# Kernel tuning notes

Hardware: AMD Instinct MI355X
Metric: run time of the kernel (lower is better)

The kernel has to match this reference:

```python
import jax, jax.numpy as jnp
import numpy as np

BATCH, SEQ, FEAT, UNITS, OUT = 128, 2048, 64, 64, 6


def setup_inputs() -> dict:
    key = jax.random.key(0)
    ks = jax.random.split(key, 12)
    s = 0.05
    inp = {
        "x": jax.random.normal(ks[0], (BATCH, SEQ, FEAT), dtype=jnp.float32),
        # LSTMCell 0 (kernel, recurrent_kernel, bias); gate order i,f,g,o
        "W0": jax.random.normal(ks[1], (FEAT, 4 * UNITS), dtype=jnp.float32) * s,
        "U0": jax.random.normal(ks[2], (UNITS, 4 * UNITS), dtype=jnp.float32) * s,
        "b0": jax.random.normal(ks[3], (4 * UNITS,), dtype=jnp.float32) * s,
        # LSTMCell 1 (shared by layers 2 AND 3, as in the original code)
        "W1": jax.random.normal(ks[4], (UNITS, 4 * UNITS), dtype=jnp.float32) * s,
        "U1": jax.random.normal(ks[5], (UNITS, 4 * UNITS), dtype=jnp.float32) * s,
        "b1": jax.random.normal(ks[6], (4 * UNITS,), dtype=jnp.float32) * s,
        # Dense heads
        "Wf": jax.random.normal(ks[7], (UNITS, 64), dtype=jnp.float32) * s,
        "bf": jax.random.normal(ks[8], (64,), dtype=jnp.float32) * s,
        "Wo": jax.random.normal(ks[9], (64, OUT), dtype=jnp.float32) * s,
        "bo": jax.random.normal(ks[10], (OUT,), dtype=jnp.float32) * s,
    }
    return inp


def _lstm_cell(c, h, xin, W, U, b):
    # Keras LSTMCell math, gate order i, f, g(candidate), o
    z = xin @ W + h @ U + b  # [B, 4U]
    i, f, g, o = jnp.split(z, 4, axis=-1)
    c_new = jax.nn.sigmoid(f) * c + jax.nn.sigmoid(i) * jnp.tanh(g)
    h_new = jax.nn.sigmoid(o) * jnp.tanh(c_new)
    return c_new, h_new


def reference(x, W0, U0, b0, W1, U1, b1, Wf, bf, Wo, bo):
    B = x.shape[0]
    z = jnp.zeros((B, UNITS), dtype=x.dtype)
    init = (z, z, z, z, z, z)  # (c0,h0,c1,h1,c2,h2)

    def step(carry, xt):
        c0, h0, c1, h1, c2, h2 = carry
        c0, h0 = _lstm_cell(c0, h0, xt, W0, U0, b0)
        c1, h1 = _lstm_cell(c1, h1, h0, W1, U1, b1)
        # NOTE: original code reuses rnn_cell1's weights for the 3rd layer
        c2, h2 = _lstm_cell(c2, h2, h1, W1, U1, b1)
        return (c0, h0, c1, h1, c2, h2), None

    xt = jnp.swapaxes(x, 0, 1)  # [T, B, F]
    (c0, h0, c1, h1, c2, h2), _ = jax.lax.scan(step, init, xt)
    y = jax.nn.relu(h2 @ Wf + bf)
    return y @ Wo + bo
```

## Files before the change

### kernel.cpp

```cpp
#include <hip/hip_runtime.h>

#define BATCHN 128
#define SEQT   2048
#define FEAT   64
#define UNITS  64
#define NCOL   256
#define OUTD   6
#define CH     24
#define BUF    96

typedef float v2f __attribute__((ext_vector_type(2)));

__device__ __forceinline__ float fast_exp2(float x) {
#if __has_builtin(__builtin_amdgcn_exp2f)
    return __builtin_amdgcn_exp2f(x);
#else
    return exp2f(x);
#endif
}
__device__ __forceinline__ float fast_rcp(float x) {
#if __has_builtin(__builtin_amdgcn_rcpf)
    return __builtin_amdgcn_rcpf(x);
#else
    return 1.0f / x;
#endif
}
__device__ __forceinline__ float sig_(float x) {
    return fast_rcp(1.0f + fast_exp2(-1.4426950408889634f * x));
}
__device__ __forceinline__ float tanh_(float x) {
    float xc = fminf(fmaxf(x, -15.0f), 15.0f);
    float e  = fast_exp2(2.8853900817779268f * xc);
    return (e - 1.0f) * fast_rcp(e + 1.0f);
}

__device__ __forceinline__ v2f pk_fma(v2f a, v2f b, v2f c) {
    return __builtin_elementwise_fma(a, b, c);
}

template<int CTRL>
__device__ __forceinline__ float dppf(float v) {
    return __builtin_bit_cast(float, __builtin_amdgcn_update_dpp(
        0, __builtin_bit_cast(int, v), CTRL, 0xF, 0xF, true));
}
__device__ __forceinline__ v2f red8v(v2f v) {
    v2f t;
    t.x = dppf<0xB1>(v.x);  t.y = dppf<0xB1>(v.y);  v = v + t;
    t.x = dppf<0x4E>(v.x);  t.y = dppf<0x4E>(v.y);  v = v + t;
    t.x = dppf<0x141>(v.x); t.y = dppf<0x141>(v.y); v = v + t;
    return v;
}

__global__ __launch_bounds__(768, 3)
void lstm3_g8p(const float* __restrict__ x,
               const float* __restrict__ W0, const float* __restrict__ U0,
               const float* __restrict__ b0,
               const float* __restrict__ W1, const float* __restrict__ U1,
               const float* __restrict__ b1,
               const float* __restrict__ Wf, const float* __restrict__ bfv,
               const float* __restrict__ Wo, const float* __restrict__ bov,
               float* __restrict__ out)
{
    const int b   = blockIdx.x;
    const int tid = threadIdx.x;
    const int grp = tid >> 8;
    const int lt  = tid & 255;
    const int cg  = lt >> 3;
    const int kg  = lt & 7;
    const int up  = kg & 1;
    const int myu = 2 * cg + up;

    __shared__ __align__(16) float ls[8 * BUF];
    __shared__ float lact[UNITS];
    float* const lsb = ls;

    const float* Wsel = (grp == 0) ? W0 : W1;
    const float* Usel = (grp == 0) ? U0 : U1;
    const float* bsel = (grp == 0) ? b0 : b1;
    const float* Msel = (kg < 4) ? Wsel : Usel;

    v2f wt[16][4];
    float biasv[4];
#pragma unroll
    for (int g = 0; g < 4; ++g) {
        const int colb = (g << 6) + 2 * cg;
#pragma unroll
        for (int k = 0; k < 16; ++k) {
            const int r = (kg & 3) * 16 + k;
            wt[k][g] = (v2f){Msel[r * NCOL + colb], Msel[r * NCOL + colb + 1]};
        }
        biasv[g] = bsel[(g << 6) + myu];
    }

    if (tid < 6 * BUF) lsb[tid] = 0.f;

    const float* xbase = x + (size_t)b * SEQT * FEAT;
    const bool xload = (grp == 0) && (lt < 16);
    float* xwp0 = lsb + 6 * BUF + CH * (lt >> 2) + 4 * (lt & 3);
    float* xwp1 = xwp0 + BUF;

    float4 xr0, xr1;
    if (xload) {
        *(float4*)xwp1 = *(const float4*)(xbase + lt * 4);
        xr0 = *(const float4*)(xbase + (size_t)1 * FEAT + lt * 4);
        xr1 = *(const float4*)(xbase + (size_t)2 * FEAT + lt * 4);
    }
    __syncthreads();

    const float* inB0 = (grp == 0) ? (lsb + 6 * BUF) : (lsb + (2 * (grp - 1)) * BUF);
    const float* inB1 = inB0 + BUF;
    const float* rcB0 = lsb + (2 * grp) * BUF;
    const float* rcB1 = rcB0 + BUF;
    const int chOff = (kg & 3) * CH;
    const float* opP0 = ((kg < 4) ? inB0 : rcB0) + chOff;
    const float* opP1 = ((kg < 4) ? inB1 : rcB1) + chOff;

    float* hwp0 = lsb + (2 * grp) * BUF + CH * (myu >> 4) + (myu & 15);
    float* hwp1 = hwp0 + BUF;

    float c = 0.f;

#define MAC1(V, K)                                                            \
    { v2f s_; s_.x = (V); s_.y = (V);                                         \
      a0 = pk_fma(s_, wt[K][0], a0);                                          \
      a1 = pk_fma(s_, wt[K][1], a1);                                          \
      a2 = pk_fma(s_, wt[K][2], a2);                                          \
      a3 = pk_fma(s_, wt[K][3], a3); }

#define TICK(TK, PUBW, XR)                                                    \
    {                                                                         \
        if (xload) {                                                          \
            *(float4*)(PUBW) = (XR);                                          \
            int tn = (TK) + 3; if (tn > SEQT - 1) tn = SEQT - 1;              \
            (XR) = *(const float4*)(xbase + (size_t)tn * FEAT + lt * 4);      \
        }                                                                     \
        const int t_ = (TK) - grp;                                            \
        if (t_ >= 0 && t_ < SEQT) {                                           \
            const float* op = ((TK) & 1) ? opP0 : opP1;   \
            float4 o0 = *(const float4*)(op);                                 \
            float4 o1 = *(const float4*)(op + 4);                             \
            float4 o2 = *(const float4*)(op + 8);                             \
            float4 o3 = *(const float4*)(op + 12);                            \
            v2f a0 = (v2f){0.f, 0.f}, a1 = a0, a2 = a0, a3 = a0;              \
            MAC1(o0.x, 0)  MAC1(o0.y, 1)  MAC1(o0.z, 2)  MAC1(o0.w, 3)        \
            MAC1(o1.x, 4)  MAC1(o1.y, 5)  MAC1(o1.z, 6)  MAC1(o1.w, 7)        \
            MAC1(o2.x, 8)  MAC1(o2.y, 9)  MAC1(o2.z, 10) MAC1(o2.w, 11)       \
            MAC1(o3.x, 12) MAC1(o3.y, 13) MAC1(o3.z, 14) MAC1(o3.w, 15)       \
            v2f z0 = red8v(a0), z1 = red8v(a1), z2 = red8v(a2), z3 = red8v(a3);\
            const float zi = (up ? z0.y : z0.x) + biasv[0];                   \
            const float zf = (up ? z1.y : z1.x) + biasv[1];                   \
            const float zg = (up ? z2.y : z2.x) + biasv[2];                   \
            const float zo = (up ? z3.y : z3.x) + biasv[3];                   \
            const float ig = sig_(zi), fg = sig_(zf);                         \
            const float gg = tanh_(zg), og = sig_(zo);                        \
            c = fg * c + ig * gg;                                             \
            const float hn = og * tanh_(c);                                   \
            if (kg < 2) *(((TK) & 1) ? hwp1 : hwp0) = hn;                     \
        }                                                                     \
        asm volatile("s_waitcnt lgkmcnt(0)\n\ts_barrier" ::: "memory");       \
    }

    for (int tk = 0; tk < SEQT + 2; tk += 2) {
        TICK(tk,     xwp0, xr0)
        TICK(tk + 1, xwp1, xr1)
    }
#undef TICK
#undef MAC1

    const float* h2f = lsb + (2 * 2 + 1) * BUF;
    if (tid < UNITS) {
        float a = bfv[tid];
#pragma unroll
        for (int k = 0; k < UNITS; ++k)
            a += h2f[CH * (k >> 4) + (k & 15)] * Wf[k * 64 + tid];
        lact[tid] = fmaxf(a, 0.f);
    }
    __syncthreads();
    if (tid < OUTD) {
        float a = bov[tid];
#pragma unroll
        for (int k = 0; k < UNITS; ++k) a += lact[k] * Wo[k * OUTD + tid];
        out[b * OUTD + tid] = a;
    }
}

extern "C" void kernel_launch(void* const* d_in, const int* in_sizes, int n_in,
                              void* d_out, int out_size, void* d_ws, size_t ws_size,
                              hipStream_t stream) {
    const float* x   = (const float*)d_in[0];
    const float* W0  = (const float*)d_in[1];
    const float* U0  = (const float*)d_in[2];
    const float* b0  = (const float*)d_in[3];
    const float* W1  = (const float*)d_in[4];
    const float* U1  = (const float*)d_in[5];
    const float* b1  = (const float*)d_in[6];
    const float* Wf  = (const float*)d_in[7];
    const float* bfv = (const float*)d_in[8];
    const float* Wo  = (const float*)d_in[9];
    const float* bov = (const float*)d_in[10];
    float* out = (float*)d_out;

    lstm3_g8p<<<BATCHN, 768, 0, stream>>>(x, W0, U0, b0, W1, U1, b1,
                                          Wf, bfv, Wo, bov, out);
}
```

Measured before the change: 2.235 ms.

## Restructure LSTM kernel to one-unit-per-lane waves with readlane broadcast

Replaces the 768-thread layout, which used an 8-way K split plus DPP reductions, with 384 threads in 6 waves. Each (layer, input/recurrent) pair gets one wave, and each lane holds a full 64-row weight column for its unit. Operands are broadcast with readlane instead of LDS vector loads, and partial sums are exchanged through LDS between the input wave and the recurrent wave. This removes the cross-lane reductions and the LDS operand reads, but it deepens the pipeline to 6 stages, serialises 64 readlanes per step and uses about 256 weight registers per lane.

```diff
diff --git a/kernel.cpp b/kernel.cpp
--- a/kernel.cpp
+++ b/kernel.cpp
@@ -6,8 +6,6 @@
 #define UNITS  64
 #define NCOL   256
 #define OUTD   6
-#define CH     24
-#define BUF    96
 
 typedef float v2f __attribute__((ext_vector_type(2)));
 
@@ -38,141 +36,113 @@
     return __builtin_elementwise_fma(a, b, c);
 }
 
-template<int CTRL>
-__device__ __forceinline__ float dppf(float v) {
-    return __builtin_bit_cast(float, __builtin_amdgcn_update_dpp(
-        0, __builtin_bit_cast(int, v), CTRL, 0xF, 0xF, true));
-}
-__device__ __forceinline__ v2f red8v(v2f v) {
-    v2f t;
-    t.x = dppf<0xB1>(v.x);  t.y = dppf<0xB1>(v.y);  v = v + t;
-    t.x = dppf<0x4E>(v.x);  t.y = dppf<0x4E>(v.y);  v = v + t;
-    t.x = dppf<0x141>(v.x); t.y = dppf<0x141>(v.y); v = v + t;
-    return v;
+__device__ __forceinline__ float rl_(float v, int l) {
+    return __builtin_bit_cast(float,
+        __builtin_amdgcn_readlane(__builtin_bit_cast(int, v), l));
 }
 
-__global__ __launch_bounds__(768, 3)
-void lstm3_g8p(const float* __restrict__ x,
-               const float* __restrict__ W0, const float* __restrict__ U0,
-               const float* __restrict__ b0,
-               const float* __restrict__ W1, const float* __restrict__ U1,
-               const float* __restrict__ b1,
-               const float* __restrict__ Wf, const float* __restrict__ bfv,
-               const float* __restrict__ Wo, const float* __restrict__ bov,
-               float* __restrict__ out)
+__global__ __launch_bounds__(384, 1)
+void lstm3_rl(const float* __restrict__ x,
+              const float* __restrict__ W0, const float* __restrict__ U0,
+              const float* __restrict__ b0,
+              const float* __restrict__ W1, const float* __restrict__ U1,
+              const float* __restrict__ b1,
+              const float* __restrict__ Wf, const float* __restrict__ bfv,
+              const float* __restrict__ Wo, const float* __restrict__ bov,
+              float* __restrict__ out)
 {
     const int b   = blockIdx.x;
     const int tid = threadIdx.x;
-    const int grp = tid >> 8;
-    const int lt  = tid & 255;
-    const int cg  = lt >> 3;
-    const int kg  = lt & 7;
-    const int up  = kg & 1;
-    const int myu = 2 * cg + up;
+    const int wid = tid >> 6;
+    const int g   = wid >> 1;
+    const int r   = wid & 1;
+    const int u   = tid & 63;
 
-    __shared__ __align__(16) float ls[8 * BUF];
+    __shared__ __align__(16) float lzff[3][2][4 * UNITS];
+    __shared__ __align__(16) float lh[3][2][UNITS];
     __shared__ float lact[UNITS];
-    float* const lsb = ls;
 
-    const float* Wsel = (grp == 0) ? W0 : W1;
-    const float* Usel = (grp == 0) ? U0 : U1;
-    const float* bsel = (grp == 0) ? b0 : b1;
-    const float* Msel = (kg < 4) ? Wsel : Usel;
+    const float* M = (g == 0) ? ((r == 0) ? W0 : U0)
+                              : ((r == 0) ? W1 : U1);
+    v2f wif[64], wgo[64];
+#pragma unroll
+    for (int k = 0; k < 64; ++k) {
+        wif[k] = (v2f){M[k * NCOL +       u], M[k * NCOL +  64 + u]};
+        wgo[k] = (v2f){M[k * NCOL + 128 + u], M[k * NCOL + 192 + u]};
+    }
+    const float* bsel = (g == 0) ? b0 : b1;
+    const v2f bif = (v2f){bsel[u],       bsel[ 64 + u]};
+    const v2f bgo = (v2f){bsel[128 + u], bsel[192 + u]};
 
-    v2f wt[16][4];
-    float biasv[4];
-#pragma unroll
-    for (int g = 0; g < 4; ++g) {
-        const int colb = (g << 6) + 2 * cg;
-#pragma unroll
-        for (int k = 0; k < 16; ++k) {
-            const int r = (kg & 3) * 16 + k;
-            wt[k][g] = (v2f){Msel[r * NCOL + colb], Msel[r * NCOL + colb + 1]};
-        }
-        biasv[g] = bsel[(g << 6) + myu];
+    for (int i = tid; i < 3 * 2 * 4 * UNITS; i += 384) ((float*)lzff)[i] = 0.f;
+    for (int i = tid; i < 3 * 2 * UNITS;     i += 384) ((float*)lh)[i]   = 0.f;
+
+    const float* xrow = x + (size_t)b * SEQT * FEAT + u;
+    const bool isX = (wid == 0);
+    float xr0 = 0.f, xr1 = 0.f;
+    if (isX) { xr0 = xrow[0]; xr1 = xrow[FEAT]; }
+    __syncthreads();
+
+    const int alpha = 2 * g + r;
+    float hreg = 0.f, creg = 0.f;
+
+#define TICK(TK, XR)                                                          \
+    {                                                                         \
+        const int p_ = (TK) & 1;                                              \
+        const int t_ = (TK) - alpha;                                          \
+        const float xcur = (XR);                                              \
+        if (isX) {                  \
+            int tn = (TK) + 2; if (tn > SEQT - 1) tn = SEQT - 1;              \
+            (XR) = xrow[(size_t)tn * FEAT];                                   \
+        }                                                                     \
+        if (t_ >= 0 && t_ < SEQT) {                                           \
+            float src;                                                        \
+            if (r == 0) src = (g == 0) ? xcur : lh[g - 1][p_ ^ 1][u];         \
+            else        src = hreg;                  \
+            v2f aifA = (r == 0) ? bif : (v2f){0.f, 0.f};                      \
+            v2f agoA = (r == 0) ? bgo : (v2f){0.f, 0.f};                      \
+            v2f aifB = (v2f){0.f, 0.f}, agoB = (v2f){0.f, 0.f};               \
+            _Pragma("unroll")                                                 \
+            for (int k = 0; k < 64; k += 2) {                                 \
+                const float h0 = rl_(src, k);                                 \
+                const float h1 = rl_(src, k + 1);                             \
+                const v2f hv0 = (v2f){h0, h0};                                \
+                const v2f hv1 = (v2f){h1, h1};                                \
+                aifA = pk_fma(hv0, wif[k],     aifA);                         \
+                agoA = pk_fma(hv0, wgo[k],     agoA);                         \
+                aifB = pk_fma(hv1, wif[k + 1], aifB);                         \
+                agoB = pk_fma(hv1, wgo[k + 1], agoB);                         \
+            }                                                                 \
+            const v2f aif = aifA + aifB;                                      \
+            const v2f ago = agoA + agoB;                                      \
+            if (r == 0) {                                                     \
+                float4 z4 = {aif.x, aif.y, ago.x, ago.y};                     \
+                *(float4*)&lzff[g][p_][4 * u] = z4;                           \
+            } else {                                                          \
+                float4 z4 = *(const float4*)&lzff[g][p_ ^ 1][4 * u];          \
+                const float zi = z4.x + aif.x, zf = z4.y + aif.y;             \
+                const float zg = z4.z + ago.x, zo = z4.w + ago.y;             \
+                const float pi = sig_(zi), pf = sig_(zf);                     \
+                const float pg = tanh_(zg), po = sig_(zo);                    \
+                creg = pf * creg + pi * pg;                                   \
+                hreg = po * tanh_(creg);                                      \
+                lh[g][p_][u] = hreg;                                          \
+            }                                                                 \
+        }                                                                     \
+        __syncthreads();                                                      \
     }
 
-    if (tid < 6 * BUF) lsb[tid] = 0.f;
-
-    const float* xbase = x + (size_t)b * SEQT * FEAT;
-    const bool xload = (grp == 0) && (lt < 16);
-    float* xwp0 = lsb + 6 * BUF + CH * (lt >> 2) + 4 * (lt & 3);
-    float* xwp1 = xwp0 + BUF;
-
-    float4 xr0, xr1;
-    if (xload) {
-        *(float4*)xwp1 = *(const float4*)(xbase + lt * 4);
-        xr0 = *(const float4*)(xbase + (size_t)1 * FEAT + lt * 4);
-        xr1 = *(const float4*)(xbase + (size_t)2 * FEAT + lt * 4);
-    }
-    __syncthreads();
-
-    const float* inB0 = (grp == 0) ? (lsb + 6 * BUF) : (lsb + (2 * (grp - 1)) * BUF);
-    const float* inB1 = inB0 + BUF;
-    const float* rcB0 = lsb + (2 * grp) * BUF;
-    const float* rcB1 = rcB0 + BUF;
-    const int chOff = (kg & 3) * CH;
-    const float* opP0 = ((kg < 4) ? inB0 : rcB0) + chOff;
-    const float* opP1 = ((kg < 4) ? inB1 : rcB1) + chOff;
-
-    float* hwp0 = lsb + (2 * grp) * BUF + CH * (myu >> 4) + (myu & 15);
-    float* hwp1 = hwp0 + BUF;
-
-    float c = 0.f;
-
-#define MAC1(V, K)                                                            \
-    { v2f s_; s_.x = (V); s_.y = (V);                                         \
-      a0 = pk_fma(s_, wt[K][0], a0);                                          \
-      a1 = pk_fma(s_, wt[K][1], a1);                                          \
-      a2 = pk_fma(s_, wt[K][2], a2);                                          \
-      a3 = pk_fma(s_, wt[K][3], a3); }
-
-#define TICK(TK, PUBW, XR)                                                    \
-    {                                                                         \
-        if (xload) {                                                          \
-            *(float4*)(PUBW) = (XR);                                          \
-            int tn = (TK) + 3; if (tn > SEQT - 1) tn = SEQT - 1;              \
-            (XR) = *(const float4*)(xbase + (size_t)tn * FEAT + lt * 4);      \
-        }                                                                     \
-        const int t_ = (TK) - grp;                                            \
-        if (t_ >= 0 && t_ < SEQT) {                                           \
-            const float* op = ((TK) & 1) ? opP0 : opP1;   \
-            float4 o0 = *(const float4*)(op);                                 \
-            float4 o1 = *(const float4*)(op + 4);                             \
-            float4 o2 = *(const float4*)(op + 8);                             \
-            float4 o3 = *(const float4*)(op + 12);                            \
-            v2f a0 = (v2f){0.f, 0.f}, a1 = a0, a2 = a0, a3 = a0;              \
-            MAC1(o0.x, 0)  MAC1(o0.y, 1)  MAC1(o0.z, 2)  MAC1(o0.w, 3)        \
-            MAC1(o1.x, 4)  MAC1(o1.y, 5)  MAC1(o1.z, 6)  MAC1(o1.w, 7)        \
-            MAC1(o2.x, 8)  MAC1(o2.y, 9)  MAC1(o2.z, 10) MAC1(o2.w, 11)       \
-            MAC1(o3.x, 12) MAC1(o3.y, 13) MAC1(o3.z, 14) MAC1(o3.w, 15)       \
-            v2f z0 = red8v(a0), z1 = red8v(a1), z2 = red8v(a2), z3 = red8v(a3);\
-            const float zi = (up ? z0.y : z0.x) + biasv[0];                   \
-            const float zf = (up ? z1.y : z1.x) + biasv[1];                   \
-            const float zg = (up ? z2.y : z2.x) + biasv[2];                   \
-            const float zo = (up ? z3.y : z3.x) + biasv[3];                   \
-            const float ig = sig_(zi), fg = sig_(zf);                         \
-            const float gg = tanh_(zg), og = sig_(zo);                        \
-            c = fg * c + ig * gg;                                             \
-            const float hn = og * tanh_(c);                                   \
-            if (kg < 2) *(((TK) & 1) ? hwp1 : hwp0) = hn;                     \
-        }                                                                     \
-        asm volatile("s_waitcnt lgkmcnt(0)\n\ts_barrier" ::: "memory");       \
-    }
-
-    for (int tk = 0; tk < SEQT + 2; tk += 2) {
-        TICK(tk,     xwp0, xr0)
-        TICK(tk + 1, xwp1, xr1)
+    for (int tk = 0; tk < SEQT + 6; tk += 2) {
+        TICK(tk,     xr0)
+        TICK(tk + 1, xr1)
     }
 #undef TICK
-#undef MAC1
 
-    const float* h2f = lsb + (2 * 2 + 1) * BUF;
+    const float* h2f = lh[2][0];
     if (tid < UNITS) {
         float a = bfv[tid];
 #pragma unroll
-        for (int k = 0; k < UNITS; ++k)
-            a += h2f[CH * (k >> 4) + (k & 15)] * Wf[k * 64 + tid];
+        for (int k = 0; k < UNITS; ++k) a += h2f[k] * Wf[k * 64 + tid];
         lact[tid] = fmaxf(a, 0.f);
     }
     __syncthreads();
@@ -200,6 +170,6 @@
     const float* bov = (const float*)d_in[10];
     float* out = (float*)d_out;
 
-    lstm3_g8p<<<BATCHN, 768, 0, stream>>>(x, W0, U0, b0, W1, U1, b1,
-                                          Wf, bfv, Wo, bov, out);
+    lstm3_rl<<<BATCHN, 384, 0, stream>>>(x, W0, U0, b0, W1, U1, b1,
+                                         Wf, bfv, Wo, bov, out);
 }
```

Measured after the change: 4.883 ms. +118.5%, slower.
